# Kernel tuning notes

Measured on AMD Instinct MI355X. Metric: run time of the kernel, lower is better.

Reference implementation:

```python
import jax, jax.numpy as jnp
import numpy as np

D_MODEL, D_STATE, D_CONV, EXPAND, N_HEADS = 768, 64, 4, 2, 12
D_INNER = D_MODEL * EXPAND           # 1536
HEAD_DIM = D_INNER // N_HEADS        # 128
IN_PROJ = D_INNER * 2 + N_HEADS * D_STATE * 2 + N_HEADS  # 4620
EPS = 1e-5


def setup_inputs() -> dict:
    key = jax.random.key(0)
    ks = jax.random.split(key, 8)
    s = lambda fan_in: 1.0 / np.sqrt(fan_in)
    return {
        "x": jax.random.normal(ks[0], (1, 1024, D_MODEL), dtype=jnp.float32),
        "W_in": jax.random.normal(ks[1], (IN_PROJ, D_MODEL), dtype=jnp.float32) * s(D_MODEL),
        "conv_w": jax.random.normal(ks[2], (D_INNER, D_CONV), dtype=jnp.float32) * s(D_CONV),
        "conv_b": jnp.zeros((D_INNER,), dtype=jnp.float32),
        "A_log": jnp.full((N_HEADS,), np.log(0.5), dtype=jnp.float32),
        "Dp": jnp.ones((N_HEADS,), dtype=jnp.float32),
        "dt_bias": jnp.zeros((N_HEADS,), dtype=jnp.float32),
        "W_out": jax.random.normal(ks[3], (D_MODEL, D_INNER), dtype=jnp.float32) * s(D_INNER),
        "norm_w": jnp.ones((D_INNER,), dtype=jnp.float32),
    }


def _causal_conv1d(x, w, b):
    # x: (B,L,Din), depthwise causal conv with kernel size D_CONV
    L = x.shape[1]
    xp = jnp.pad(x, ((0, 0), (D_CONV - 1, 0), (0, 0)))
    y = b
    for i in range(D_CONV):  # fixed small kernel, unrolled
        y = y + xp[:, i:i + L, :] * w[:, i]
    return y


def reference(x, W_in, conv_w, conv_b, A_log, Dp, dt_bias, W_out, norm_w):
    B_sz, L, _ = x.shape
    nh, ds, hd = N_HEADS, D_STATE, HEAD_DIM
    proj = jnp.einsum('bld,pd->blp', x, W_in)
    z = proj[:, :, :D_INNER]
    x_ssm = proj[:, :, D_INNER:2 * D_INNER]
    o = 2 * D_INNER
    Bm = proj[:, :, o:o + nh * ds].reshape(B_sz, L, nh, ds)
    Cm = proj[:, :, o + nh * ds:o + 2 * nh * ds].reshape(B_sz, L, nh, ds)
    dt_r = proj[:, :, o + 2 * nh * ds:]
    dt = jax.nn.softplus(dt_r) + dt_bias[None, None, :]          # (B,L,nh)

    x_ssm = jax.nn.silu(_causal_conv1d(x_ssm, conv_w, conv_b))
    x_ssm = x_ssm.reshape(B_sz, L, nh, hd)

    A = -jnp.exp(A_log)                                          # (nh,)
    log_decay = A[None, None, :] * dt                            # (B,L,nh)
    Phi = jnp.cumsum(log_decay, axis=1)
    dB = dt[..., None] * Bm                                      # (B,L,nh,ds)
    # b: (B,L,nh,hd,ds) outer product
    b = dB[:, :, :, None, :] * x_ssm[..., None]
    max_exp = 80.0
    exp_neg_Phi = jnp.exp(jnp.minimum(-Phi, max_exp))[..., None, None]
    b_cumsum = jnp.cumsum(exp_neg_Phi * b, axis=1)
    h = jnp.exp(Phi)[..., None, None] * b_cumsum                 # (B,L,nh,hd,ds)
    y = jnp.sum(Cm[:, :, :, None, :] * h, axis=-1)               # (B,L,nh,hd)
    y = y + Dp[None, None, :, None] * x_ssm
    y = y.reshape(B_sz, L, D_INNER)

    # RMSNorm then gate
    rms = jax.lax.rsqrt(jnp.mean(y * y, axis=-1, keepdims=True) + EPS)
    y = y * rms * norm_w
    y = y * jax.nn.silu(z)
    return jnp.einsum('bli,di->bld', y, W_out)
```

## Files before the change

kernel.cpp:

```cpp
#include <hip/hip_runtime.h>
#include <cmath>

#define LSEQ   1024
#define NPROJ  4620
#define NPADW  4736
#define DINNER 1536
#define NH     12
#define HDIM   128
#define OFF_Z  0
#define OFF_X  1536
#define OFF_B  3072
#define OFF_C  3840
#define OFF_DT 4608

typedef unsigned short u16;
typedef unsigned int u32;
typedef short bf16x8 __attribute__((ext_vector_type(8)));
typedef float f32x4 __attribute__((ext_vector_type(4)));

__device__ inline u16 f2b(float f) {
  unsigned u = __float_as_uint(f);
  return (u16)((u + 0x7fffu + ((u >> 16) & 1u)) >> 16);
}
__device__ inline float b2f(u16 h) { return __uint_as_float(((unsigned)h) << 16); }
__device__ inline u32 pk2(float a, float b) { return (u32)f2b(a) | ((u32)f2b(b) << 16); }

__device__ inline void gll16(const void* g, void* l) {
  __builtin_amdgcn_global_load_lds((const __attribute__((address_space(1))) void*)g,
                                   (__attribute__((address_space(3))) void*)l, 16, 0, 0);
}

#define S0N 196608
#define S1N 909312
#define S1V 887040
#define S2N 294912
__global__ __launch_bounds__(256) void ksplit_all(const float* __restrict__ x,
    const float* __restrict__ Wi, const float* __restrict__ Wo,
    u16* __restrict__ Ah, u16* __restrict__ Wh, u16* __restrict__ Woh) {
  int i = blockIdx.x * 256 + threadIdx.x;
  const float* src; u16* hi; int j, valid;
  if (i < S0N)            { src = x;  hi = Ah;  j = i;              valid = S0N; }
  else if (i < S0N + S1N) { src = Wi; hi = Wh;  j = i - S0N;        valid = S1V; }
  else                    { src = Wo; hi = Woh; j = i - S0N - S1N;  valid = S2N; }
  float4 v = (j < valid) ? ((const float4*)src)[j] : make_float4(0.f, 0.f, 0.f, 0.f);
  ((uint2*)hi)[j] = make_uint2(pk2(v.x, v.y), pk2(v.z, v.w));
}

template<int BM, int BN, int MAP, bool NG>
__global__ __launch_bounds__(256) void gemm1(const u16* __restrict__ Ah,
    const u16* __restrict__ Wh, float* __restrict__ C,
    int lda, int ldw, int Ksl, int Nreal, int ldc) {
  constexpr int PLA = BM * 64;
  constexpr int IA = BM / 8, IW = BN / 8, ITOT = IA + IW;
  constexpr int FRn = BN / 32;
  __shared__ u16 lds[PLA + BN * 64];
  const int tid = threadIdx.x;
  const int l = tid & 63, w = tid >> 6;
  const int wm = w >> 1, wn = w & 1;
  const int kg = l >> 4, li = l & 15;

  int b = blockIdx.x, m0, n0, koff;
  float* Cp = C;
  if (MAP == 0) {
    int xcd = b & 7, idx = b >> 3;
    m0 = (idx & 15) * 64;
    n0 = (xcd * 5 + (idx >> 4)) * 128;
    koff = 0;
    if (NG && n0 >= NPADW) return;
  } else {
    int xcd = b & 7, idx = b >> 3;
    int gg = xcd * 6 + (idx >> 4);
    m0 = (idx & 15) * 64;
    n0 = (gg % 12) * 64;
    koff = (gg / 12) * 384;
    Cp = C + (size_t)(gg / 12) * LSEQ * ldc;
  }

  const int srcg = ((l & 7) ^ (l >> 3)) * 8;
  auto stage = [&](int t) {
    const int k0 = koff + t * 64;
    for (int q = w; q < ITOT; q += 4) {
      const u16* gb; int r0b, ldk, dst;
      if (q < IA) { gb = Ah; r0b = m0 + 8 * q;        dst = 8 * q * 64;              ldk = lda; }
      else        { gb = Wh; r0b = n0 + 8 * (q - IA); dst = PLA + 8 * (q - IA) * 64; ldk = ldw; }
      gll16(gb + (size_t)(r0b + (l >> 3)) * ldk + k0 + srcg, &lds[dst]);
    }
  };
  auto rd = [&](int region, int row, int ks) -> bf16x8 {
    return *(const bf16x8*)&lds[region + row * 64 + (((ks * 4 + kg) ^ (row & 7)) << 3)];
  };

  f32x4 acc[2][FRn];
#pragma unroll
  for (int m = 0; m < 2; ++m)
#pragma unroll
    for (int n = 0; n < FRn; ++n) acc[m][n] = (f32x4){0.f, 0.f, 0.f, 0.f};

  const int NT = Ksl / 64;
  stage(0);
  asm volatile("s_waitcnt vmcnt(0)" ::: "memory");
  __syncthreads();
  for (int t = 0; t < NT; ++t) {
    bf16x8 af[2][2], wf[FRn][2];
#pragma unroll
    for (int ks = 0; ks < 2; ++ks) {
#pragma unroll
      for (int m = 0; m < 2; ++m)
        af[m][ks] = rd(0, wm * 32 + m * 16 + li, ks);
#pragma unroll
      for (int n = 0; n < FRn; ++n)
        wf[n][ks] = rd(PLA, wn * (BN / 2) + n * 16 + li, ks);
    }
    __syncthreads();
    if (t + 1 < NT) stage(t + 1);
#pragma unroll
    for (int ks = 0; ks < 2; ++ks)
#pragma unroll
      for (int m = 0; m < 2; ++m)
#pragma unroll
        for (int n = 0; n < FRn; ++n)
          acc[m][n] = __builtin_amdgcn_mfma_f32_16x16x32_bf16(af[m][ks], wf[n][ks], acc[m][n], 0, 0, 0);
    if (t + 1 < NT) {
      asm volatile("s_waitcnt vmcnt(0)" ::: "memory");
      __syncthreads();
    }
  }
#pragma unroll
  for (int m = 0; m < 2; ++m) {
    int rbase = m0 + wm * 32 + m * 16 + kg * 4;
#pragma unroll
    for (int n = 0; n < FRn; ++n) {
      int col = n0 + wn * (BN / 2) + n * 16 + li;
      if (!NG || col < Nreal) {
#pragma unroll
        for (int r = 0; r < 4; ++r)
          Cp[(size_t)(rbase + r) * ldc + col] = acc[m][n][r];
      }
    }
  }
}

__global__ __launch_bounds__(256) void addk(const float* __restrict__ P,
    float* __restrict__ out) {
  const int S = LSEQ * 768 / 4;
  int i = blockIdx.x * 256 + threadIdx.x;
  float4 a = ((const float4*)P)[i];
  float4 b = ((const float4*)P)[i + S];
  float4 c = ((const float4*)P)[i + 2 * S];
  float4 d = ((const float4*)P)[i + 3 * S];
  ((float4*)out)[i] = make_float4(a.x + b.x + c.x + d.x, a.y + b.y + c.y + d.y,
                                  a.z + b.z + c.z + d.z, a.w + b.w + c.w + d.w);
}

__global__ __launch_bounds__(256) void dtphi(const float* __restrict__ proj,
    const float* __restrict__ A_log, const float* __restrict__ dt_bias,
    float* __restrict__ Phi, float* __restrict__ dts) {
  int h = blockIdx.x, tid = threadIdx.x;
  float Ac = -expf(A_log[h]);
  float bb = dt_bias[h];
  float v[4], s = 0.f;
#pragma unroll
  for (int u = 0; u < 4; ++u) {
    int t = tid * 4 + u;
    float xr = proj[(size_t)t * NPROJ + OFF_DT + h];
    float sp = (xr > 20.f) ? xr : log1pf(expf(xr));
    v[u] = sp + bb;
    s += v[u];
  }
  int lane = tid & 63, wv = tid >> 6;
  float ps = s;
#pragma unroll
  for (int d = 1; d < 64; d <<= 1) {
    float o = __shfl_up(ps, d);
    if (lane >= d) ps += o;
  }
  __shared__ float wsum[4];
  if (lane == 63) wsum[wv] = ps;
  __syncthreads();
  float off = 0.f;
  for (int w = 0; w < wv; ++w) off += wsum[w];
  float run = off + ps - s;
#pragma unroll
  for (int u = 0; u < 4; ++u) {
    int t = tid * 4 + u;
    run += v[u];
    Phi[t * NH + h] = Ac * run;
    dts[t * NH + h] = v[u];
  }
}

__global__ __launch_bounds__(256) void conv_state(const float* __restrict__ proj,
    const float* __restrict__ cw, const float* __restrict__ cb,
    const float* __restrict__ Phi, const float* __restrict__ dts,
    u16* __restrict__ xactT, float* __restrict__ SlocF) {
  const int k = blockIdx.x, h = blockIdx.y, tid = threadIdx.x;
  const int l = tid & 63, w = tid >> 6, kg = l >> 4, li = l & 15;
  __shared__ u16 Bw[64 * 64];
  __shared__ u16 Xt[128 * 64];
  __shared__ float wS[64];
  const int s0 = k * 64;
  if (tid < 64) {
    float pe = Phi[(s0 + 63) * NH + h];
    float p  = Phi[(s0 + tid) * NH + h];
    wS[tid] = expf(pe + fminf(-p, 80.f)) * dts[(s0 + tid) * NH + h];
  }
  __syncthreads();
#pragma unroll
  for (int u = 0; u < 4; ++u) {
    int idx = tid + u * 256, s = idx >> 4, q = (idx & 15) * 4;
    float4 v = *(const float4*)(proj + (size_t)(s0 + s) * NPROJ + OFF_B + h * 64 + q);
    float ws_ = wS[s];
    float vv[4] = {v.x, v.y, v.z, v.w};
#pragma unroll
    for (int j = 0; j < 4; ++j) {
      int d = q + j;
      Bw[d * 64 + (((s >> 3) ^ (d & 7)) << 3) + (s & 7)] = f2b(vv[j] * ws_);
    }
  }
  {
    int c = tid & 127, th = tid >> 7;
    int cg = h * HDIM + c;
    float w0 = cw[cg * 4], w1 = cw[cg * 4 + 1], w2 = cw[cg * 4 + 2], w3 = cw[cg * 4 + 3];
    float bias = cb[cg];
    int tb = s0 + th * 32;
    auto P = [&](int t) { return (t >= 0) ? proj[(size_t)t * NPROJ + OFF_X + cg] : 0.f; };
    float x0 = P(tb - 3), x1 = P(tb - 2), x2 = P(tb - 1);
    u32 pkb[16];
    float prev = 0.f;
#pragma unroll
    for (int i = 0; i < 32; ++i) {
      float x3 = P(tb + i);
      float a = bias;
      a = fmaf(x0, w0, a); a = fmaf(x1, w1, a); a = fmaf(x2, w2, a); a = fmaf(x3, w3, a);
      float sv = a / (1.f + expf(-a));
      if (i & 1) pkb[i >> 1] = pk2(prev, sv); else prev = sv;
      x0 = x1; x1 = x2; x2 = x3;
    }
#pragma unroll
    for (int g = 0; g < 4; ++g) {
      int sg = th * 4 + g;
      *(uint4*)&Xt[c * 64 + ((sg ^ (c & 7)) << 3)] =
          make_uint4(pkb[g * 4], pkb[g * 4 + 1], pkb[g * 4 + 2], pkb[g * 4 + 3]);
    }
    size_t xo = ((size_t)(k * NH + h) * 128 + c) * 64 + th * 32;
#pragma unroll
    for (int g = 0; g < 4; ++g)
      *(uint4*)(xactT + xo + g * 8) =
          make_uint4(pkb[g * 4], pkb[g * 4 + 1], pkb[g * 4 + 2], pkb[g * 4 + 3]);
  }
  __syncthreads();
  const int wm = w >> 1, wn = w & 1;
  auto rd = [&](const u16* reg, int row, int ks) -> bf16x8 {
    return *(const bf16x8*)&reg[row * 64 + (((ks * 4 + kg) ^ (row & 7)) << 3)];
  };
  f32x4 acc[4][2];
#pragma unroll
  for (int m = 0; m < 4; ++m)
#pragma unroll
    for (int n = 0; n < 2; ++n) acc[m][n] = (f32x4){0.f, 0.f, 0.f, 0.f};
#pragma unroll
  for (int ks = 0; ks < 2; ++ks) {
    bf16x8 xf[4], bf[2];
#pragma unroll
    for (int m = 0; m < 4; ++m) xf[m] = rd(Xt, wm * 64 + m * 16 + li, ks);
#pragma unroll
    for (int n = 0; n < 2; ++n) bf[n] = rd(Bw, wn * 32 + n * 16 + li, ks);
#pragma unroll
    for (int m = 0; m < 4; ++m)
#pragma unroll
      for (int n = 0; n < 2; ++n)
        acc[m][n] = __builtin_amdgcn_mfma_f32_16x16x32_bf16(xf[m], bf[n], acc[m][n], 0, 0, 0);
  }
  float* dst = SlocF + ((size_t)(k * NH + h) << 13);
#pragma unroll
  for (int m = 0; m < 4; ++m)
#pragma unroll
    for (int n = 0; n < 2; ++n)
#pragma unroll
      for (int r = 0; r < 4; ++r) {
        int c = wm * 64 + m * 16 + kg * 4 + r;
        int d = wn * 32 + n * 16 + li;
        dst[c * 64 + d] = acc[m][n][r];
      }
}

__global__ __launch_bounds__(256) void chunk_scan(const float* __restrict__ SlocF,
    u16* __restrict__ SlocT, const float* __restrict__ Phi) {
  int b = blockIdx.x;
  int h = b >> 5;
  int e = (b & 31) * 256 + threadIdx.x;
  float run = SlocF[((size_t)h << 13) + e];
  SlocT[((size_t)h << 13) + e] = f2b(run);
#pragma unroll
  for (int k = 1; k < 16; ++k) {
    float lam = expf(Phi[(k * 64 + 63) * NH + h] - Phi[(k * 64 - 1) * NH + h]);
    size_t o = ((size_t)(k * NH + h) << 13) + e;
    run = fmaf(lam, run, SlocF[o]);
    SlocT[o] = f2b(run);
  }
}

__global__ __launch_bounds__(256) void ssm_out(const float* __restrict__ proj,
    const u16* __restrict__ xactT, const float* __restrict__ Phi,
    const float* __restrict__ dts, const float* __restrict__ Dp,
    const u16* __restrict__ SlocT, u16* __restrict__ ybuf) {
  const int k = blockIdx.x, h = blockIdx.y, zh = blockIdx.z, tid = threadIdx.x;
  const int l = tid & 63, w = tid >> 6, kg = l >> 4, li = l & 15;
  const int wm = w >> 1, wn = w & 1;
  __shared__ u16 Cs[4096], Bs[4096], Ps[4096], Xs[4096], Ss[4096];
  __shared__ float phiT[64], eSs[64], dSs[64], eTs[64];
  const int t0 = k * 64;
  const int srcg = ((l & 7) ^ (l >> 3)) * 8;
  {
    const u16* xsrc = xactT + ((size_t)(k * NH + h) * 128 + zh * 64) * 64;
#pragma unroll
    for (int j = 0; j < 2; ++j) {
      int rb = w * 16 + j * 8;
      gll16(xsrc + (size_t)(rb + (l >> 3)) * 64 + srcg, &Xs[rb * 64]);
    }
    if (k > 0) {
      const u16* ssrc = SlocT + (((size_t)((k - 1) * NH + h)) << 13) + (size_t)(zh * 64) * 64;
#pragma unroll
      for (int j = 0; j < 2; ++j) {
        int rb = w * 16 + j * 8;
        gll16(ssrc + (size_t)(rb + (l >> 3)) * 64 + srcg, &Ss[rb * 64]);
      }
    }
  }
#pragma unroll
  for (int u = 0; u < 4; ++u) {
    int idx = tid + u * 256, i = idx >> 4, q = (idx & 15) * 4;
    int aoff = i * 64 + (((q >> 3) ^ (i & 7)) << 3) + (q & 4);
    float4 cv = *(const float4*)(proj + (size_t)(t0 + i) * NPROJ + OFF_C + h * 64 + q);
    float4 bv = *(const float4*)(proj + (size_t)(t0 + i) * NPROJ + OFF_B + h * 64 + q);
    *(uint2*)&Cs[aoff] = make_uint2(pk2(cv.x, cv.y), pk2(cv.z, cv.w));
    *(uint2*)&Bs[aoff] = make_uint2(pk2(bv.x, bv.y), pk2(bv.z, bv.w));
  }
  if (tid < 64) {
    float p = Phi[(t0 + tid) * NH + h];
    phiT[tid] = p;
    eSs[tid] = fminf(-p, 80.f);
    dSs[tid] = dts[(t0 + tid) * NH + h];
    eTs[tid] = (k > 0) ? expf(p - Phi[(t0 - 1) * NH + h]) : 0.f;
  }
  __syncthreads();
  auto rd = [&](const u16* reg, int row, int ks) -> bf16x8 {
    return *(const bf16x8*)&reg[row * 64 + (((ks * 4 + kg) ^ (row & 7)) << 3)];
  };
  bf16x8 Cf[2][2];
  f32x4 accS[2][2];
#pragma unroll
  for (int m = 0; m < 2; ++m)
#pragma unroll
    for (int n = 0; n < 2; ++n) accS[m][n] = (f32x4){0.f, 0.f, 0.f, 0.f};
#pragma unroll
  for (int ks = 0; ks < 2; ++ks) {
    bf16x8 Bf[2];
#pragma unroll
    for (int m = 0; m < 2; ++m) Cf[m][ks] = rd(Cs, wm * 32 + m * 16 + li, ks);
#pragma unroll
    for (int n = 0; n < 2; ++n) Bf[n] = rd(Bs, wn * 32 + n * 16 + li, ks);
#pragma unroll
    for (int m = 0; m < 2; ++m)
#pragma unroll
      for (int n = 0; n < 2; ++n)
        accS[m][n] = __builtin_amdgcn_mfma_f32_16x16x32_bf16(Cf[m][ks], Bf[n], accS[m][n], 0, 0, 0);
  }
#pragma unroll
  for (int m = 0; m < 2; ++m)
#pragma unroll
    for (int n = 0; n < 2; ++n)
#pragma unroll
      for (int r = 0; r < 4; ++r) {
        int t = wm * 32 + m * 16 + kg * 4 + r;
        int s = wn * 32 + n * 16 + li;
        float f = (s <= t) ? expf(phiT[t] + eSs[s]) * dSs[s] : 0.f;
        Ps[t * 64 + (((s >> 3) ^ (t & 7)) << 3) + (s & 7)] = f2b(accS[m][n][r] * f);
      }
  __syncthreads();
  f32x4 accY[2][2], acc2[2][2];
#pragma unroll
  for (int m = 0; m < 2; ++m)
#pragma unroll
    for (int n = 0; n < 2; ++n) {
      accY[m][n] = (f32x4){0.f, 0.f, 0.f, 0.f};
      acc2[m][n] = (f32x4){0.f, 0.f, 0.f, 0.f};
    }
#pragma unroll
  for (int ks = 0; ks < 2; ++ks) {
    bf16x8 Pf[2], Xf[2];
#pragma unroll
    for (int m = 0; m < 2; ++m) Pf[m] = rd(Ps, wm * 32 + m * 16 + li, ks);
#pragma unroll
    for (int n = 0; n < 2; ++n) Xf[n] = rd(Xs, wn * 32 + n * 16 + li, ks);
#pragma unroll
    for (int m = 0; m < 2; ++m)
#pragma unroll
      for (int n = 0; n < 2; ++n)
        accY[m][n] = __builtin_amdgcn_mfma_f32_16x16x32_bf16(Pf[m], Xf[n], accY[m][n], 0, 0, 0);
    if (k > 0) {
      bf16x8 Sf[2];
#pragma unroll
      for (int n = 0; n < 2; ++n) Sf[n] = rd(Ss, wn * 32 + n * 16 + li, ks);
#pragma unroll
      for (int m = 0; m < 2; ++m)
#pragma unroll
        for (int n = 0; n < 2; ++n)
          acc2[m][n] = __builtin_amdgcn_mfma_f32_16x16x32_bf16(Cf[m][ks], Sf[n], acc2[m][n], 0, 0, 0);
    }
  }
  float dp = Dp[h];
#pragma unroll
  for (int m = 0; m < 2; ++m)
#pragma unroll
    for (int n = 0; n < 2; ++n)
#pragma unroll
      for (int r = 0; r < 4; ++r) {
        int t = wm * 32 + m * 16 + kg * 4 + r;
        int c = wn * 32 + n * 16 + li;
        float xv = b2f(Xs[c * 64 + (((t >> 3) ^ (c & 7)) << 3) + (t & 7)]);
        float val = accY[m][n][r] + eTs[t] * acc2[m][n][r] + dp * xv;
        ybuf[(size_t)(t0 + t) * DINNER + h * HDIM + zh * 64 + c] = f2b(val);
      }
}

__global__ __launch_bounds__(256) void norm_gate(const u16* __restrict__ y,
    const float* __restrict__ proj, const float* __restrict__ nw,
    u16* __restrict__ yh) {
  int t = blockIdx.x, tid = threadIdx.x;
  float v[6], ss = 0.f;
#pragma unroll
  for (int k = 0; k < 6; ++k) {
    v[k] = b2f(y[(size_t)t * DINNER + tid + k * 256]);
    ss = fmaf(v[k], v[k], ss);
  }
#pragma unroll
  for (int d = 1; d < 64; d <<= 1) ss += __shfl_xor(ss, d);
  __shared__ float wsum[4];
  int wv = tid >> 6;
  if ((tid & 63) == 0) wsum[wv] = ss;
  __syncthreads();
  float tot = wsum[0] + wsum[1] + wsum[2] + wsum[3];
  float rms = rsqrtf(tot / 1536.f + 1e-5f);
#pragma unroll
  for (int k = 0; k < 6; ++k) {
    int c = tid + k * 256;
    float z = proj[(size_t)t * NPROJ + OFF_Z + c];
    float sz = z / (1.f + expf(-z));
    yh[(size_t)t * DINNER + c] = f2b(v[k] * rms * nw[c] * sz);
  }
}

extern "C" void kernel_launch(void* const* d_in, const int* in_sizes, int n_in,
                              void* d_out, int out_size, void* d_ws, size_t ws_size,
                              hipStream_t stream) {
  const float* x       = (const float*)d_in[0];
  const float* W_in    = (const float*)d_in[1];
  const float* conv_w  = (const float*)d_in[2];
  const float* conv_b  = (const float*)d_in[3];
  const float* A_log   = (const float*)d_in[4];
  const float* Dp      = (const float*)d_in[5];
  const float* dt_bias = (const float*)d_in[6];
  const float* W_out   = (const float*)d_in[7];
  const float* norm_w  = (const float*)d_in[8];
  float* out = (float*)d_out;

  char* base = (char*)d_ws;
  size_t o = 0;
  auto alloc = [&](size_t bytes) { char* r = base + o; o += (bytes + 255) & ~(size_t)255; return r; };
  float* proj  = (float*)alloc((size_t)LSEQ * NPROJ * 4);
  u16*   ybuf  = (u16*)alloc((size_t)LSEQ * DINNER * 2);
  float* Phi   = (float*)alloc((size_t)LSEQ * NH * 4);
  float* dtsb  = (float*)alloc((size_t)LSEQ * NH * 4);
  float* SlocF = (float*)alloc((size_t)16 * NH * 8192 * 4);
  u16*   SlocT = (u16*)alloc((size_t)16 * NH * 8192 * 2);
  u16*   xactT = (u16*)alloc((size_t)16 * NH * 128 * 64 * 2);
  u16* Ah  = (u16*)alloc((size_t)LSEQ * 768 * 2);
  u16* Wh  = (u16*)alloc((size_t)NPADW * 768 * 2);
  u16* Woh = (u16*)alloc((size_t)768 * DINNER * 2);
  u16* Yh  = (u16*)alloc((size_t)LSEQ * DINNER * 2);
  float* Pp = proj;

  ksplit_all<<<dim3((S0N + S1N + S2N) / 256), 256, 0, stream>>>(
      x, W_in, W_out, Ah, Wh, Woh);
  gemm1<64, 128, 0, true><<<dim3(640), 256, 0, stream>>>(
      Ah, Wh, proj, 768, 768, 768, NPROJ, NPROJ);
  dtphi<<<dim3(NH), 256, 0, stream>>>(proj, A_log, dt_bias, Phi, dtsb);
  conv_state<<<dim3(16, NH), 256, 0, stream>>>(proj, conv_w, conv_b, Phi, dtsb, xactT, SlocF);
  chunk_scan<<<dim3(NH * 32), 256, 0, stream>>>(SlocF, SlocT, Phi);
  ssm_out<<<dim3(16, NH, 2), 256, 0, stream>>>(proj, xactT, Phi, dtsb, Dp, SlocT, ybuf);
  norm_gate<<<dim3(LSEQ), 256, 0, stream>>>(ybuf, proj, norm_w, Yh);
  gemm1<64, 64, 1, false><<<dim3(768), 256, 0, stream>>>(
      Yh, Woh, Pp, 1536, 1536, 384, 768, 768);
  addk<<<dim3(LSEQ * 768 / 4 / 256), 256, 0, stream>>>(Pp, out);
}
```

Measured before the change: 72.25 us.

## Store projection in bf16, double-buffer GEMM LDS, fold chunk scan into ssm_out

The input projection GEMM now writes its output as bf16 instead of fp32, with a separate fp32 copy of the dt columns so the softplus/cumsum stays in full precision. Downstream kernels read bf16 directly, and ssm_out loads C and B tiles with async global-to-LDS copies. The GEMM moves to double-buffered LDS, issuing the next tile's loads before the current MFMAs instead of waiting on them. The separate chunk_scan kernel is removed: conv_state writes per-chunk states in bf16 and ssm_out forms the inter-chunk state as a decay-weighted sum over all previous chunks. This cuts one launch and halves projection traffic, at the cost of O(k) redundant reads in later chunks and lower precision for the B, C, x and z values.

```diff
diff --git a/kernel.cpp b/kernel.cpp
--- a/kernel.cpp
+++ b/kernel.cpp
@@ -46,21 +46,21 @@
   ((uint2*)hi)[j] = make_uint2(pk2(v.x, v.y), pk2(v.z, v.w));
 }
 
-template<int BM, int BN, int MAP, bool NG>
+template<int BM, int BN, int MAP, bool NG, bool OBF>
 __global__ __launch_bounds__(256) void gemm1(const u16* __restrict__ Ah,
-    const u16* __restrict__ Wh, float* __restrict__ C,
+    const u16* __restrict__ Wh, void* __restrict__ Cv, float* __restrict__ dtr,
     int lda, int ldw, int Ksl, int Nreal, int ldc) {
   constexpr int PLA = BM * 64;
-  constexpr int IA = BM / 8, IW = BN / 8, ITOT = IA + IW;
+  constexpr int PB = PLA + BN * 64;
+  constexpr int IA = BM / 8, ITOT = IA + BN / 8;
   constexpr int FRn = BN / 32;
-  __shared__ u16 lds[PLA + BN * 64];
+  __shared__ u16 lds[2 * PB];
   const int tid = threadIdx.x;
   const int l = tid & 63, w = tid >> 6;
   const int wm = w >> 1, wn = w & 1;
   const int kg = l >> 4, li = l & 15;
 
-  int b = blockIdx.x, m0, n0, koff;
-  float* Cp = C;
+  int b = blockIdx.x, m0, n0, koff, cslice = 0;
   if (MAP == 0) {
     int xcd = b & 7, idx = b >> 3;
     m0 = (idx & 15) * 64;
@@ -73,21 +73,21 @@
     m0 = (idx & 15) * 64;
     n0 = (gg % 12) * 64;
     koff = (gg / 12) * 384;
-    Cp = C + (size_t)(gg / 12) * LSEQ * ldc;
+    cslice = gg / 12;
   }
 
   const int srcg = ((l & 7) ^ (l >> 3)) * 8;
-  auto stage = [&](int t) {
+  auto stage = [&](int buf, int t) {
     const int k0 = koff + t * 64;
     for (int q = w; q < ITOT; q += 4) {
       const u16* gb; int r0b, ldk, dst;
       if (q < IA) { gb = Ah; r0b = m0 + 8 * q;        dst = 8 * q * 64;              ldk = lda; }
       else        { gb = Wh; r0b = n0 + 8 * (q - IA); dst = PLA + 8 * (q - IA) * 64; ldk = ldw; }
-      gll16(gb + (size_t)(r0b + (l >> 3)) * ldk + k0 + srcg, &lds[dst]);
+      gll16(gb + (size_t)(r0b + (l >> 3)) * ldk + k0 + srcg, &lds[buf * PB + dst]);
     }
   };
-  auto rd = [&](int region, int row, int ks) -> bf16x8 {
-    return *(const bf16x8*)&lds[region + row * 64 + (((ks * 4 + kg) ^ (row & 7)) << 3)];
+  auto rd = [&](int buf, int region, int row, int ks) -> bf16x8 {
+    return *(const bf16x8*)&lds[buf * PB + region + row * 64 + (((ks * 4 + kg) ^ (row & 7)) << 3)];
   };
 
   f32x4 acc[2][FRn];
@@ -97,22 +97,21 @@
     for (int n = 0; n < FRn; ++n) acc[m][n] = (f32x4){0.f, 0.f, 0.f, 0.f};
 
   const int NT = Ksl / 64;
-  stage(0);
-  asm volatile("s_waitcnt vmcnt(0)" ::: "memory");
-  __syncthreads();
+  stage(0, 0);
+  __syncthreads();
+  int buf = 0;
   for (int t = 0; t < NT; ++t) {
+    if (t + 1 < NT) stage(buf ^ 1, t + 1);
     bf16x8 af[2][2], wf[FRn][2];
 #pragma unroll
     for (int ks = 0; ks < 2; ++ks) {
 #pragma unroll
       for (int m = 0; m < 2; ++m)
-        af[m][ks] = rd(0, wm * 32 + m * 16 + li, ks);
+        af[m][ks] = rd(buf, 0, wm * 32 + m * 16 + li, ks);
 #pragma unroll
       for (int n = 0; n < FRn; ++n)
-        wf[n][ks] = rd(PLA, wn * (BN / 2) + n * 16 + li, ks);
-    }
-    __syncthreads();
-    if (t + 1 < NT) stage(t + 1);
+        wf[n][ks] = rd(buf, PLA, wn * (BN / 2) + n * 16 + li, ks);
+    }
 #pragma unroll
     for (int ks = 0; ks < 2; ++ks)
 #pragma unroll
@@ -120,10 +119,8 @@
 #pragma unroll
         for (int n = 0; n < FRn; ++n)
           acc[m][n] = __builtin_amdgcn_mfma_f32_16x16x32_bf16(af[m][ks], wf[n][ks], acc[m][n], 0, 0, 0);
-    if (t + 1 < NT) {
-      asm volatile("s_waitcnt vmcnt(0)" ::: "memory");
-      __syncthreads();
-    }
+    __syncthreads();
+    buf ^= 1;
   }
 #pragma unroll
   for (int m = 0; m < 2; ++m) {
@@ -133,8 +130,15 @@
       int col = n0 + wn * (BN / 2) + n * 16 + li;
       if (!NG || col < Nreal) {
 #pragma unroll
-        for (int r = 0; r < 4; ++r)
-          Cp[(size_t)(rbase + r) * ldc + col] = acc[m][n][r];
+        for (int r = 0; r < 4; ++r) {
+          if (OBF) ((u16*)Cv)[(size_t)(rbase + r) * ldc + col] = f2b(acc[m][n][r]);
+          else ((float*)Cv)[(size_t)(cslice * LSEQ + rbase + r) * ldc + col] = acc[m][n][r];
+        }
+        if (MAP == 0 && col >= OFF_DT) {
+#pragma unroll
+          for (int r = 0; r < 4; ++r)
+            dtr[(size_t)(rbase + r) * NH + (col - OFF_DT)] = acc[m][n][r];
+        }
       }
     }
   }
@@ -152,7 +156,7 @@
                                   a.z + b.z + c.z + d.z, a.w + b.w + c.w + d.w);
 }
 
-__global__ __launch_bounds__(256) void dtphi(const float* __restrict__ proj,
+__global__ __launch_bounds__(256) void dtphi(const float* __restrict__ dtraw,
     const float* __restrict__ A_log, const float* __restrict__ dt_bias,
     float* __restrict__ Phi, float* __restrict__ dts) {
   int h = blockIdx.x, tid = threadIdx.x;
@@ -162,7 +166,7 @@
 #pragma unroll
   for (int u = 0; u < 4; ++u) {
     int t = tid * 4 + u;
-    float xr = proj[(size_t)t * NPROJ + OFF_DT + h];
+    float xr = dtraw[(size_t)t * NH + h];
     float sp = (xr > 20.f) ? xr : log1pf(expf(xr));
     v[u] = sp + bb;
     s += v[u];
@@ -189,14 +193,14 @@
   }
 }
 
-__global__ __launch_bounds__(256) void conv_state(const float* __restrict__ proj,
+__global__ __launch_bounds__(256) void conv_state(const u16* __restrict__ proj,
     const float* __restrict__ cw, const float* __restrict__ cb,
     const float* __restrict__ Phi, const float* __restrict__ dts,
-    u16* __restrict__ xactT, float* __restrict__ SlocF) {
+    u16* __restrict__ xactT, u16* __restrict__ Sloc) {
   const int k = blockIdx.x, h = blockIdx.y, tid = threadIdx.x;
   const int l = tid & 63, w = tid >> 6, kg = l >> 4, li = l & 15;
-  __shared__ u16 Bw[64 * 64];
-  __shared__ u16 Xt[128 * 64];
+  __shared__ u16 Bw[4096];
+  __shared__ u16 Xt[8192];
   __shared__ float wS[64];
   const int s0 = k * 64;
   if (tid < 64) {
@@ -206,15 +210,17 @@
   }
   __syncthreads();
 #pragma unroll
-  for (int u = 0; u < 4; ++u) {
-    int idx = tid + u * 256, s = idx >> 4, q = (idx & 15) * 4;
-    float4 v = *(const float4*)(proj + (size_t)(s0 + s) * NPROJ + OFF_B + h * 64 + q);
+  for (int u = 0; u < 2; ++u) {
+    int idx = tid + u * 256;
+    int s = idx >> 3, dq = (idx & 7) * 8;
+    uint4 rw = *(const uint4*)(proj + (size_t)(s0 + s) * NPROJ + OFF_B + h * 64 + dq);
     float ws_ = wS[s];
-    float vv[4] = {v.x, v.y, v.z, v.w};
-#pragma unroll
-    for (int j = 0; j < 4; ++j) {
-      int d = q + j;
-      Bw[d * 64 + (((s >> 3) ^ (d & 7)) << 3) + (s & 7)] = f2b(vv[j] * ws_);
+    u32 pk[4] = {rw.x, rw.y, rw.z, rw.w};
+#pragma unroll
+    for (int j = 0; j < 8; ++j) {
+      float bv = b2f((u16)(pk[j >> 1] >> ((j & 1) * 16)));
+      int d = dq + j;
+      Bw[d * 64 + (((s >> 3) ^ (d & 7)) << 3) + (s & 7)] = f2b(bv * ws_);
     }
   }
   {
@@ -223,7 +229,7 @@
     float w0 = cw[cg * 4], w1 = cw[cg * 4 + 1], w2 = cw[cg * 4 + 2], w3 = cw[cg * 4 + 3];
     float bias = cb[cg];
     int tb = s0 + th * 32;
-    auto P = [&](int t) { return (t >= 0) ? proj[(size_t)t * NPROJ + OFF_X + cg] : 0.f; };
+    auto P = [&](int t) { return (t >= 0) ? b2f(proj[(size_t)t * NPROJ + OFF_X + cg]) : 0.f; };
     float x0 = P(tb - 3), x1 = P(tb - 2), x2 = P(tb - 1);
     u32 pkb[16];
     float prev = 0.f;
@@ -271,7 +277,7 @@
       for (int n = 0; n < 2; ++n)
         acc[m][n] = __builtin_amdgcn_mfma_f32_16x16x32_bf16(xf[m], bf[n], acc[m][n], 0, 0, 0);
   }
-  float* dst = SlocF + ((size_t)(k * NH + h) << 13);
+  u16* dst = Sloc + (((size_t)(k * NH + h)) << 13);
 #pragma unroll
   for (int m = 0; m < 4; ++m)
 #pragma unroll
@@ -280,61 +286,29 @@
       for (int r = 0; r < 4; ++r) {
         int c = wm * 64 + m * 16 + kg * 4 + r;
         int d = wn * 32 + n * 16 + li;
-        dst[c * 64 + d] = acc[m][n][r];
+        dst[c * 64 + d] = f2b(acc[m][n][r]);
       }
 }
 
-__global__ __launch_bounds__(256) void chunk_scan(const float* __restrict__ SlocF,
-    u16* __restrict__ SlocT, const float* __restrict__ Phi) {
-  int b = blockIdx.x;
-  int h = b >> 5;
-  int e = (b & 31) * 256 + threadIdx.x;
-  float run = SlocF[((size_t)h << 13) + e];
-  SlocT[((size_t)h << 13) + e] = f2b(run);
-#pragma unroll
-  for (int k = 1; k < 16; ++k) {
-    float lam = expf(Phi[(k * 64 + 63) * NH + h] - Phi[(k * 64 - 1) * NH + h]);
-    size_t o = ((size_t)(k * NH + h) << 13) + e;
-    run = fmaf(lam, run, SlocF[o]);
-    SlocT[o] = f2b(run);
-  }
-}
-
-__global__ __launch_bounds__(256) void ssm_out(const float* __restrict__ proj,
+__global__ __launch_bounds__(256) void ssm_out(const u16* __restrict__ proj,
     const u16* __restrict__ xactT, const float* __restrict__ Phi,
     const float* __restrict__ dts, const float* __restrict__ Dp,
-    const u16* __restrict__ SlocT, u16* __restrict__ ybuf) {
+    const u16* __restrict__ Sloc, u16* __restrict__ ybuf) {
   const int k = blockIdx.x, h = blockIdx.y, zh = blockIdx.z, tid = threadIdx.x;
   const int l = tid & 63, w = tid >> 6, kg = l >> 4, li = l & 15;
   const int wm = w >> 1, wn = w & 1;
   __shared__ u16 Cs[4096], Bs[4096], Ps[4096], Xs[4096], Ss[4096];
-  __shared__ float phiT[64], eSs[64], dSs[64], eTs[64];
+  __shared__ float phiT[64], eSs[64], dSs[64], eTs[64], wJ[16];
   const int t0 = k * 64;
   const int srcg = ((l & 7) ^ (l >> 3)) * 8;
-  {
-    const u16* xsrc = xactT + ((size_t)(k * NH + h) * 128 + zh * 64) * 64;
-#pragma unroll
-    for (int j = 0; j < 2; ++j) {
-      int rb = w * 16 + j * 8;
-      gll16(xsrc + (size_t)(rb + (l >> 3)) * 64 + srcg, &Xs[rb * 64]);
-    }
-    if (k > 0) {
-      const u16* ssrc = SlocT + (((size_t)((k - 1) * NH + h)) << 13) + (size_t)(zh * 64) * 64;
-#pragma unroll
-      for (int j = 0; j < 2; ++j) {
-        int rb = w * 16 + j * 8;
-        gll16(ssrc + (size_t)(rb + (l >> 3)) * 64 + srcg, &Ss[rb * 64]);
-      }
-    }
-  }
-#pragma unroll
-  for (int u = 0; u < 4; ++u) {
-    int idx = tid + u * 256, i = idx >> 4, q = (idx & 15) * 4;
-    int aoff = i * 64 + (((q >> 3) ^ (i & 7)) << 3) + (q & 4);
-    float4 cv = *(const float4*)(proj + (size_t)(t0 + i) * NPROJ + OFF_C + h * 64 + q);
-    float4 bv = *(const float4*)(proj + (size_t)(t0 + i) * NPROJ + OFF_B + h * 64 + q);
-    *(uint2*)&Cs[aoff] = make_uint2(pk2(cv.x, cv.y), pk2(cv.z, cv.w));
-    *(uint2*)&Bs[aoff] = make_uint2(pk2(bv.x, bv.y), pk2(bv.z, bv.w));
+  for (int q = w; q < 24; q += 4) {
+    int rb = (q & 7) * 8;
+    if (q < 8)
+      gll16(proj + (size_t)(t0 + rb + (l >> 3)) * NPROJ + OFF_C + h * 64 + srcg, &Cs[rb * 64]);
+    else if (q < 16)
+      gll16(proj + (size_t)(t0 + rb + (l >> 3)) * NPROJ + OFF_B + h * 64 + srcg, &Bs[rb * 64]);
+    else
+      gll16(xactT + ((size_t)(k * NH + h) * 128 + zh * 64 + rb + (l >> 3)) * 64 + srcg, &Xs[rb * 64]);
   }
   if (tid < 64) {
     float p = Phi[(t0 + tid) * NH + h];
@@ -343,6 +317,9 @@
     dSs[tid] = dts[(t0 + tid) * NH + h];
     eTs[tid] = (k > 0) ? expf(p - Phi[(t0 - 1) * NH + h]) : 0.f;
   }
+  if (tid < 16)
+    wJ[tid] = (k > 0 && tid < k)
+        ? expf(Phi[(k * 64 - 1) * NH + h] - Phi[(tid * 64 + 63) * NH + h]) : 0.f;
   __syncthreads();
   auto rd = [&](const u16* reg, int row, int ks) -> bf16x8 {
     return *(const bf16x8*)&reg[row * 64 + (((ks * 4 + kg) ^ (row & 7)) << 3)];
@@ -365,6 +342,25 @@
 #pragma unroll
       for (int n = 0; n < 2; ++n)
         accS[m][n] = __builtin_amdgcn_mfma_f32_16x16x32_bf16(Cf[m][ks], Bf[n], accS[m][n], 0, 0, 0);
+  }
+  if (k > 0) {
+    float a16[16] = {};
+    const int e0 = tid * 16;
+    for (int j = 0; j < k; ++j) {
+      const u16* sp = Sloc + (((size_t)(j * NH + h) * 128 + zh * 64) << 6) + e0;
+      uint4 ra = *(const uint4*)sp;
+      uint4 rb2 = *(const uint4*)(sp + 8);
+      float wj = wJ[j];
+      u32 pk[8] = {ra.x, ra.y, ra.z, ra.w, rb2.x, rb2.y, rb2.z, rb2.w};
+#pragma unroll
+      for (int i = 0; i < 16; ++i)
+        a16[i] = fmaf(wj, b2f((u16)(pk[i >> 1] >> ((i & 1) * 16))), a16[i]);
+    }
+#pragma unroll
+    for (int i = 0; i < 16; ++i) {
+      int e = e0 + i, c = e >> 6, d = e & 63;
+      Ss[c * 64 + (((d >> 3) ^ (c & 7)) << 3) + (d & 7)] = f2b(a16[i]);
+    }
   }
 #pragma unroll
   for (int m = 0; m < 2; ++m)
@@ -425,7 +421,7 @@
 }
 
 __global__ __launch_bounds__(256) void norm_gate(const u16* __restrict__ y,
-    const float* __restrict__ proj, const float* __restrict__ nw,
+    const u16* __restrict__ proj, const float* __restrict__ nw,
     u16* __restrict__ yh) {
   int t = blockIdx.x, tid = threadIdx.x;
   float v[6], ss = 0.f;
@@ -445,7 +441,7 @@
 #pragma unroll
   for (int k = 0; k < 6; ++k) {
     int c = tid + k * 256;
-    float z = proj[(size_t)t * NPROJ + OFF_Z + c];
+    float z = b2f(proj[(size_t)t * NPROJ + OFF_Z + c]);
     float sz = z / (1.f + expf(-z));
     yh[(size_t)t * DINNER + c] = f2b(v[k] * rms * nw[c] * sz);
   }
@@ -468,29 +464,28 @@
   char* base = (char*)d_ws;
   size_t o = 0;
   auto alloc = [&](size_t bytes) { char* r = base + o; o += (bytes + 255) & ~(size_t)255; return r; };
-  float* proj  = (float*)alloc((size_t)LSEQ * NPROJ * 4);
+  u16*   proj  = (u16*)alloc((size_t)LSEQ * NPROJ * 2);
+  float* dtraw = (float*)alloc((size_t)LSEQ * NH * 4);
+  float* Phi   = (float*)alloc((size_t)LSEQ * NH * 4);
+  float* dts   = (float*)alloc((size_t)LSEQ * NH * 4);
+  u16*   Sloc  = (u16*)alloc((size_t)16 * NH * 8192 * 2);
+  u16*   xactT = (u16*)alloc((size_t)16 * NH * 8192 * 2);
   u16*   ybuf  = (u16*)alloc((size_t)LSEQ * DINNER * 2);
-  float* Phi   = (float*)alloc((size_t)LSEQ * NH * 4);
-  float* dtsb  = (float*)alloc((size_t)LSEQ * NH * 4);
-  float* SlocF = (float*)alloc((size_t)16 * NH * 8192 * 4);
-  u16*   SlocT = (u16*)alloc((size_t)16 * NH * 8192 * 2);
-  u16*   xactT = (u16*)alloc((size_t)16 * NH * 128 * 64 * 2);
-  u16* Ah  = (u16*)alloc((size_t)LSEQ * 768 * 2);
-  u16* Wh  = (u16*)alloc((size_t)NPADW * 768 * 2);
-  u16* Woh = (u16*)alloc((size_t)768 * DINNER * 2);
-  u16* Yh  = (u16*)alloc((size_t)LSEQ * DINNER * 2);
-  float* Pp = proj;
+  u16*   Ah    = (u16*)alloc((size_t)LSEQ * 768 * 2);
+  u16*   Wh    = (u16*)alloc((size_t)NPADW * 768 * 2);
+  u16*   Woh   = (u16*)alloc((size_t)768 * DINNER * 2);
+  u16*   Yh    = (u16*)alloc((size_t)LSEQ * DINNER * 2);
+  float* Pp    = (float*)alloc((size_t)4 * LSEQ * 768 * 4);
 
   ksplit_all<<<dim3((S0N + S1N + S2N) / 256), 256, 0, stream>>>(
       x, W_in, W_out, Ah, Wh, Woh);
-  gemm1<64, 128, 0, true><<<dim3(640), 256, 0, stream>>>(
-      Ah, Wh, proj, 768, 768, 768, NPROJ, NPROJ);
-  dtphi<<<dim3(NH), 256, 0, stream>>>(proj, A_log, dt_bias, Phi, dtsb);
-  conv_state<<<dim3(16, NH), 256, 0, stream>>>(proj, conv_w, conv_b, Phi, dtsb, xactT, SlocF);
-  chunk_scan<<<dim3(NH * 32), 256, 0, stream>>>(SlocF, SlocT, Phi);
-  ssm_out<<<dim3(16, NH, 2), 256, 0, stream>>>(proj, xactT, Phi, dtsb, Dp, SlocT, ybuf);
+  gemm1<64, 128, 0, true, true><<<dim3(640), 256, 0, stream>>>(
+      Ah, Wh, proj, dtraw, 768, 768, 768, NPROJ, NPROJ);
+  dtphi<<<dim3(NH), 256, 0, stream>>>(dtraw, A_log, dt_bias, Phi, dts);
+  conv_state<<<dim3(16, NH), 256, 0, stream>>>(proj, conv_w, conv_b, Phi, dts, xactT, Sloc);
+  ssm_out<<<dim3(16, NH, 2), 256, 0, stream>>>(proj, xactT, Phi, dts, Dp, Sloc, ybuf);
   norm_gate<<<dim3(LSEQ), 256, 0, stream>>>(ybuf, proj, norm_w, Yh);
-  gemm1<64, 64, 1, false><<<dim3(768), 256, 0, stream>>>(
-      Yh, Woh, Pp, 1536, 1536, 384, 768, 768);
+  gemm1<64, 64, 1, false, false><<<dim3(768), 256, 0, stream>>>(
+      Yh, Woh, Pp, nullptr, 1536, 1536, 384, 768, 768);
   addk<<<dim3(LSEQ * 768 / 4 / 256), 256, 0, stream>>>(Pp, out);
 }
```

Result: slower. 74.90 us (+3.7%).
